# Optimization experiments

Measured on AMD Instinct MI355X. Metric: run time of the kernel, lower is better.

The kernel has to match this reference:

```python
import jax, jax.numpy as jnp
import numpy as np

N = 1_000_000   # posts
D = 256         # embedding dim
T = 5           # trait labels
U = 16384       # users (all ids assumed present; see notes)


def setup_inputs() -> dict:
    key = jax.random.key(0)
    k1, k2, k3 = jax.random.split(key, 3)
    z = jax.random.normal(k1, (N, D), dtype=jnp.float32)
    user_ids = jax.random.randint(k2, (N,), 0, U, dtype=jnp.int64)
    y = jax.random.uniform(k3, (N, T), dtype=jnp.float32)
    return {"z": z, "user_ids": user_ids, "y": y}


def reference(z, user_ids, y):
    # group-by-user mean of z and thresholded mean of y, users sorted by id
    seg = user_ids.astype(jnp.int32)
    counts = jax.ops.segment_sum(jnp.ones((seg.shape[0],), z.dtype), seg, num_segments=U)
    denom = jnp.maximum(counts, 1.0)[:, None]          # [U, 1]
    agg_z = jax.ops.segment_sum(z, seg, num_segments=U) / denom   # [U, D]
    mean_y = jax.ops.segment_sum(y, seg, num_segments=U) / denom  # [U, T]
    agg_y = (mean_y >= 0.5).astype(z.dtype)
    return agg_z, agg_y
```

## Files before the change

kernel.cpp:

```cpp
#include <hip/hip_runtime.h>

#define NPOSTS 1000000
#define DIM    256
#define TLAB   5
#define NUSERS 16384
#define SLOTS  192

__global__ void init_cursor_kernel(int* __restrict__ cursor) {
    const int u = blockIdx.x * blockDim.x + threadIdx.x;
    if (u < NUSERS) cursor[u] = u * SLOTS;
}

__global__ void scatter4_kernel(const int4* __restrict__ ids4,
                                int* __restrict__ cursor,
                                int* __restrict__ sorted, int n4) {
    const int i = blockIdx.x * blockDim.x + threadIdx.x;
    if (i < n4) {
        const int4 v = ids4[i];
        const int b = i * 4;
        sorted[atomicAdd(&cursor[v.x], 1)] = b;
        sorted[atomicAdd(&cursor[v.y], 1)] = b + 1;
        sorted[atomicAdd(&cursor[v.z], 1)] = b + 2;
        sorted[atomicAdd(&cursor[v.w], 1)] = b + 3;
    }
}

__global__ __launch_bounds__(256) void agg_kernel(const float* __restrict__ z,
                                                  const float* __restrict__ y,
                                                  const int* __restrict__ sorted,
                                                  const int* __restrict__ cursor,
                                                  float* __restrict__ out_z,
                                                  float* __restrict__ out_y) {
    const int u    = blockIdx.x;
    const int t    = threadIdx.x;
    const int w    = __builtin_amdgcn_readfirstlane(t >> 6);
    const int lane = t & 63;
    const int start = u * SLOTS;
    const int c     = cursor[u] - start;

    const int* sp = sorted + start + w;
    const int nw  = (c > w) ? ((c - w + 3) >> 2) : 0;
    const size_t col = (size_t)(lane * 4);

    float4 acc = make_float4(0.f, 0.f, 0.f, 0.f);
    float  yacc = 0.f;

    int k = 0;
    for (; k + 4 <= nw; k += 4) {
        const int i0 = sp[4 * k + 0];
        const int i1 = sp[4 * k + 4];
        const int i2 = sp[4 * k + 8];
        const int i3 = sp[4 * k + 12];
        const float4 v0 = *reinterpret_cast<const float4*>(z + (size_t)i0 * DIM + col);
        const float4 v1 = *reinterpret_cast<const float4*>(z + (size_t)i1 * DIM + col);
        const float4 v2 = *reinterpret_cast<const float4*>(z + (size_t)i2 * DIM + col);
        const float4 v3 = *reinterpret_cast<const float4*>(z + (size_t)i3 * DIM + col);
        if (lane < TLAB) {
            yacc += y[(size_t)i0 * TLAB + lane] + y[(size_t)i1 * TLAB + lane]
                  + y[(size_t)i2 * TLAB + lane] + y[(size_t)i3 * TLAB + lane];
        }
        acc.x += (v0.x + v1.x) + (v2.x + v3.x);
        acc.y += (v0.y + v1.y) + (v2.y + v3.y);
        acc.z += (v0.z + v1.z) + (v2.z + v3.z);
        acc.w += (v0.w + v1.w) + (v2.w + v3.w);
    }
    for (; k < nw; ++k) {
        const int i0 = sp[4 * k];
        const float4 v0 = *reinterpret_cast<const float4*>(z + (size_t)i0 * DIM + col);
        if (lane < TLAB) yacc += y[(size_t)i0 * TLAB + lane];
        acc.x += v0.x; acc.y += v0.y; acc.z += v0.z; acc.w += v0.w;
    }

    __shared__ float shz[4][DIM];
    __shared__ float shy[4][TLAB];
    *reinterpret_cast<float4*>(&shz[w][col]) = acc;
    if (lane < TLAB) shy[w][lane] = yacc;
    __syncthreads();

    const float denom = (c > 0) ? (float)c : 1.0f;
    const float s = (shz[0][t] + shz[1][t]) + (shz[2][t] + shz[3][t]);
    out_z[(size_t)u * DIM + t] = s / denom;
    if (t < TLAB) {
        const float ys = (shy[0][t] + shy[1][t]) + (shy[2][t] + shy[3][t]);
        out_y[(size_t)u * TLAB + t] = ((ys / denom) >= 0.5f) ? 1.0f : 0.0f;
    }
}

extern "C" void kernel_launch(void* const* d_in, const int* in_sizes, int n_in,
                              void* d_out, int out_size, void* d_ws, size_t ws_size,
                              hipStream_t stream) {
    const float* z   = (const float*)d_in[0];
    const int*   ids = (const int*)d_in[1];
    const float* y   = (const float*)d_in[2];

    const int n = in_sizes[1];

    int* sorted = (int*)d_ws;
    int* cursor = sorted + (size_t)NUSERS * SLOTS;

    float* out_z = (float*)d_out;
    float* out_y = out_z + (size_t)NUSERS * DIM;

    init_cursor_kernel<<<NUSERS / 256, 256, 0, stream>>>(cursor);

    const int n4 = n / 4;
    scatter4_kernel<<<(n4 + 255) / 256, 256, 0, stream>>>(
        (const int4*)ids, cursor, sorted, n4);

    agg_kernel<<<NUSERS, 256, 0, stream>>>(z, y, sorted, cursor, out_z, out_y);
}
```

Measured before the change: 259.1 us.

## Pad user slot lists with row 0 to drop tail loop and use contiguous chunks

The sorted workspace is zeroed, so unused slots point to row 0. Each user's count is rounded up to a multiple of 16 and each wave takes a contiguous quarter of the slots. The loop is fully unrolled by four with no remainder loop, and the padding contribution (pads times row 0 of z and y) is subtracted afterwards. This removes the tail loop and strided index reads, at the cost of a memset of the whole workspace and some redundant loads of row 0. Subtracting the padding can also introduce floating-point cancellation error.

```diff
diff --git a/kernel.cpp b/kernel.cpp
--- a/kernel.cpp
+++ b/kernel.cpp
@@ -36,21 +36,21 @@
     const int w    = __builtin_amdgcn_readfirstlane(t >> 6);
     const int lane = t & 63;
     const int start = u * SLOTS;
-    const int c     = cursor[u] - start;
+    const int c      = cursor[u] - start;
+    const int padded = (c + 15) & ~15;
+    const int q      = padded >> 2;
 
-    const int* sp = sorted + start + w;
-    const int nw  = (c > w) ? ((c - w + 3) >> 2) : 0;
+    const int* sp = sorted + start + w * q;
     const size_t col = (size_t)(lane * 4);
 
     float4 acc = make_float4(0.f, 0.f, 0.f, 0.f);
     float  yacc = 0.f;
 
-    int k = 0;
-    for (; k + 4 <= nw; k += 4) {
-        const int i0 = sp[4 * k + 0];
-        const int i1 = sp[4 * k + 4];
-        const int i2 = sp[4 * k + 8];
-        const int i3 = sp[4 * k + 12];
+    for (int k = 0; k < q; k += 4) {
+        const int i0 = sp[k + 0];
+        const int i1 = sp[k + 1];
+        const int i2 = sp[k + 2];
+        const int i3 = sp[k + 3];
         const float4 v0 = *reinterpret_cast<const float4*>(z + (size_t)i0 * DIM + col);
         const float4 v1 = *reinterpret_cast<const float4*>(z + (size_t)i1 * DIM + col);
         const float4 v2 = *reinterpret_cast<const float4*>(z + (size_t)i2 * DIM + col);
@@ -64,12 +64,6 @@
         acc.z += (v0.z + v1.z) + (v2.z + v3.z);
         acc.w += (v0.w + v1.w) + (v2.w + v3.w);
     }
-    for (; k < nw; ++k) {
-        const int i0 = sp[4 * k];
-        const float4 v0 = *reinterpret_cast<const float4*>(z + (size_t)i0 * DIM + col);
-        if (lane < TLAB) yacc += y[(size_t)i0 * TLAB + lane];
-        acc.x += v0.x; acc.y += v0.y; acc.z += v0.z; acc.w += v0.w;
-    }
 
     __shared__ float shz[4][DIM];
     __shared__ float shy[4][TLAB];
@@ -77,11 +71,15 @@
     if (lane < TLAB) shy[w][lane] = yacc;
     __syncthreads();
 
+    const int   pads  = padded - c;
+    const float fpads = (float)pads;
     const float denom = (c > 0) ? (float)c : 1.0f;
-    const float s = (shz[0][t] + shz[1][t]) + (shz[2][t] + shz[3][t]);
+    float s = (shz[0][t] + shz[1][t]) + (shz[2][t] + shz[3][t]);
+    s -= fpads * z[t];
     out_z[(size_t)u * DIM + t] = s / denom;
     if (t < TLAB) {
-        const float ys = (shy[0][t] + shy[1][t]) + (shy[2][t] + shy[3][t]);
+        float ys = (shy[0][t] + shy[1][t]) + (shy[2][t] + shy[3][t]);
+        ys -= fpads * y[t];
         out_y[(size_t)u * TLAB + t] = ((ys / denom) >= 0.5f) ? 1.0f : 0.0f;
     }
 }
@@ -101,6 +99,7 @@
     float* out_z = (float*)d_out;
     float* out_y = out_z + (size_t)NUSERS * DIM;
 
+    hipMemsetAsync(sorted, 0, (size_t)NUSERS * SLOTS * sizeof(int), stream);
     init_cursor_kernel<<<NUSERS / 256, 256, 0, stream>>>(cursor);
 
     const int n4 = n / 4;
```

New measurement: 261.7 us. Within noise of the previous version (+1.0%).
